# Performance work log

Hardware: AMD Instinct MI355X
Metric: run time of the kernel (lower is better)

Reference implementation:

```python
import jax, jax.numpy as jnp
import numpy as np

B, L, H, HKV, D, E = 2, 2048, 8, 1, 256, 2048
SCALING = D ** -0.5


def rotate_half(x):
    x1, x2 = jnp.split(x, 2, axis=-1)
    return jnp.concatenate([-x2, x1], axis=-1)


def setup_inputs() -> dict:
    key = jax.random.key(0)
    ks = jax.random.split(key, 5)
    hidden_states = jax.random.normal(ks[0], (B, L, E), jnp.float32)
    attention_mask = jnp.zeros((B, 1, 1, L, L), jnp.float32)  # additive mask (all visible)
    # standard RoPE tables, shape [L, D]
    inv_freq = 1.0 / (10000.0 ** (jnp.arange(0, D, 2, dtype=jnp.float32) / D))
    freqs = jnp.arange(L, dtype=jnp.float32)[:, None] * inv_freq[None, :]
    emb = jnp.concatenate([freqs, freqs], axis=-1)
    cos, sin = jnp.cos(emb), jnp.sin(emb)
    s = 0.02
    Wq = jax.random.normal(ks[1], (H * D, E), jnp.float32) * s
    Wk = jax.random.normal(ks[2], (HKV * D, E), jnp.float32) * s
    Wv = jax.random.normal(ks[3], (HKV * D, E), jnp.float32) * s
    Wo = jax.random.normal(ks[4], (E, H * D), jnp.float32) * s
    return {"hidden_states": hidden_states, "attention_mask": attention_mask,
            "cos": cos, "sin": sin, "Wq": Wq, "Wk": Wk, "Wv": Wv, "Wo": Wo}


def reference(hidden_states, attention_mask, cos, sin, Wq, Wk, Wv, Wo):
    b, l, _ = hidden_states.shape
    q = jnp.einsum('ble,de->bld', hidden_states, Wq)
    k = jnp.einsum('ble,de->bld', hidden_states, Wk)
    v = jnp.einsum('ble,de->bld', hidden_states, Wv)
    # q: [B, L, 1, H, D] -> transpose(1,3) -> [B, H, 1, L, D]
    q = jnp.transpose(q.reshape(b, l, 1, H, D), (0, 3, 2, 1, 4))
    # k, v: [B, 1, L, Hkv, D] -> transpose(2,3) -> [B, 1, Hkv, L, D]
    k = jnp.transpose(k.reshape(b, 1, l, HKV, D), (0, 1, 3, 2, 4))
    v = jnp.transpose(v.reshape(b, 1, l, HKV, D), (0, 1, 3, 2, 4))
    # RoPE (cos/sin broadcast over leading dims)
    q = q * cos + rotate_half(q) * sin
    k = k * cos + rotate_half(k) * sin
    # scores: [B, H, Hkv, L, L]
    attn = jnp.matmul(q, jnp.swapaxes(k, -1, -2)) * SCALING
    attn = attn + attention_mask
    attn = jax.nn.softmax(attn.astype(jnp.float32), axis=-1)
    out = jnp.matmul(attn, v)                         # [B, H, Hkv, L, D]
    out = jnp.transpose(out, (0, 1, 3, 2, 4))         # [B, H, L, Hkv, D]
    out = out.reshape(b, l, H * D)                    # row-major reshape, as torch .reshape
    return jnp.einsum('bld,ed->ble', out, Wo)
```

## Files before the change

### kernel.cpp

```cpp
#include <hip/hip_runtime.h>

typedef unsigned short u16;
typedef __attribute__((ext_vector_type(8))) short short8;
typedef __attribute__((ext_vector_type(4))) float f32x4;
typedef __attribute__((ext_vector_type(16))) float f32x16;

struct __align__(8) US4 { u16 x, y, z, w; };

__device__ __forceinline__ u16 f2bf(float x) {
  union { float f; unsigned u; } c; c.f = x;
  unsigned r = c.u + 0x7fffu + ((c.u >> 16) & 1u);
  return (u16)(r >> 16);
}
__device__ __forceinline__ float bf2f(u16 u) {
  union { unsigned u; float f; } c; c.u = ((unsigned)u) << 16;
  return c.f;
}
__device__ __forceinline__ void gload_lds16(const void* g, void* l) {
  __builtin_amdgcn_global_load_lds(
      (const __attribute__((address_space(1))) void*)g,
      (__attribute__((address_space(3))) void*)l, 16, 0, 0);
}
__device__ __forceinline__ f32x4 fzero4() {
  f32x4 z; z[0] = 0.f; z[1] = 0.f; z[2] = 0.f; z[3] = 0.f; return z;
}
__device__ __forceinline__ unsigned cvtpk(float lo, float hi) {
  unsigned r;
  asm("v_cvt_pk_bf16_f32 %0, %1, %2" : "=v"(r) : "v"(lo), "v"(hi));
  return r;
}

__global__ __launch_bounds__(256) void cvt_all(
    const float* __restrict__ h, const float* __restrict__ wq,
    const float* __restrict__ wk, const float* __restrict__ wv,
    const float* __restrict__ wo, u16* __restrict__ Xbf,
    u16* __restrict__ Wqkv, u16* __restrict__ Wob) {
  int b = blockIdx.x;
  const float* s; u16* d; int off;
  if (b < 8192)       { s = h;  d = Xbf;            off = b; }
  else if (b < 12288) { s = wq; d = Wqkv;           off = b - 8192; }
  else if (b < 12800) { s = wk; d = Wqkv + 4194304; off = b - 12288; }
  else if (b < 13312) { s = wv; d = Wqkv + 4718592; off = b - 12800; }
  else                { s = wo; d = Wob;            off = b - 13312; }
  int i = (off * 256 + threadIdx.x) * 4;
  float4 v = *(const float4*)(s + i);
  US4 o = { f2bf(v.x), f2bf(v.y), f2bf(v.z), f2bf(v.w) };
  *(US4*)(d + i) = o;
}

template <int MODE>
__global__ __launch_bounds__(256) void gemm_nt(
    const u16* __restrict__ A, const u16* __restrict__ Bw,
    u16* __restrict__ q_out, u16* __restrict__ k_out, u16* __restrict__ v_out,
    float* __restrict__ c_out) {
  __shared__ u16 lA[128 * 32];
  __shared__ u16 lB[128 * 32];
  const int K = 2048;
  int t = threadIdx.x, w = t >> 6, lane = t & 63;
  int wm = w >> 1, wn = w & 1;

  int gx = gridDim.x;
  int wg = blockIdx.y * gx + blockIdx.x;
  int per = (gx * gridDim.y) >> 3;
  int nid = (wg & 7) * per + (wg >> 3);
  int m0 = (nid % gx) * 128, n0 = (nid / gx) * 128;

  int g = lane >> 4, qi = lane & 15;

  f32x4 acc[4][4];
#pragma unroll
  for (int i = 0; i < 4; i++)
#pragma unroll
    for (int j = 0; j < 4; j++) acc[i][j] = fzero4();

  for (int k0 = 0; k0 < K; k0 += 32) {
#pragma unroll
    for (int i = 0; i < 2; i++) {
      int off = i * 4096 + w * 1024 + lane * 16;
      int row = off >> 6, cg = (off >> 4) & 3;
      gload_lds16(A + (size_t)(m0 + row) * K + k0 + cg * 8,
                  (char*)lA + i * 4096 + w * 1024);
      gload_lds16(Bw + (size_t)(n0 + row) * K + k0 + cg * 8,
                  (char*)lB + i * 4096 + w * 1024);
    }
    __syncthreads();
    short8 af[4], bfr[4];
#pragma unroll
    for (int f = 0; f < 4; f++) {
      int ra = wm * 64 + f * 16 + qi;
      int rb = wn * 64 + f * 16 + qi;
      int kb2 = g * 16;
      af[f] = *(const short8*)((const char*)lA + ra * 64 + kb2);
      bfr[f] = *(const short8*)((const char*)lB + rb * 64 + kb2);
    }
#pragma unroll
    for (int i = 0; i < 4; i++)
#pragma unroll
      for (int j = 0; j < 4; j++)
        acc[i][j] = __builtin_amdgcn_mfma_f32_16x16x32_bf16(af[i], bfr[j], acc[i][j], 0, 0, 0);
    __syncthreads();
  }

#pragma unroll
  for (int i = 0; i < 4; i++) {
#pragma unroll
    for (int j = 0; j < 4; j++) {
#pragma unroll
      for (int r = 0; r < 4; r++) {
        int m = m0 + wm * 64 + i * 16 + g * 4 + r;
        int n = n0 + wn * 64 + j * 16 + qi;
        float v = acc[i][j][r];
        if (MODE == 0) {
          int b = m >> 11, l = m & 2047;
          if (n < 2048) {
            int hh = n >> 8, dd = n & 255;
            q_out[(((size_t)(b * 8 + hh) * 2048) + l) * 256 + dd] = f2bf(v);
          } else if (n < 2304) {
            int dd = n - 2048;
            k_out[((size_t)b * 2048 + l) * 256 + dd] = f2bf(v);
          } else {
            int dd = n - 2304;
            v_out[((size_t)b * 256 + dd) * 2048 + l] = f2bf(v);
          }
        } else {
          c_out[(size_t)m * 2048 + n] = v;
        }
      }
    }
  }
}

__global__ __launch_bounds__(256) void rope_kernel(u16* __restrict__ q, u16* __restrict__ k,
                                                   const float* __restrict__ cosT,
                                                   const float* __restrict__ sinT) {
  int idx = blockIdx.x * 2 + (threadIdx.x >> 7);
  int d = threadIdx.x & 127;
  u16* ptr;
  int l;
  float sc;
  if (idx < 32768) { ptr = q + (size_t)idx * 256; l = idx & 2047; sc = 0.0625f; }
  else             { ptr = k + (size_t)(idx - 32768) * 256; l = (idx - 32768) & 2047; sc = 1.0f; }
  float x1 = bf2f(ptr[d]), x2 = bf2f(ptr[d + 128]);
  float c1 = cosT[l * 256 + d], s1 = sinT[l * 256 + d];
  float c2 = cosT[l * 256 + d + 128], s2 = sinT[l * 256 + d + 128];
  float o1 = (x1 * c1 - x2 * s1) * sc;
  float o2 = (x2 * c2 + x1 * s2) * sc;
  ptr[d] = f2bf(o1);
  ptr[d + 128] = f2bf(o2);
}

__global__ __launch_bounds__(256, 2) void flash_kernel(
    const u16* __restrict__ qr, const u16* __restrict__ kr,
    const u16* __restrict__ vt_g, u16* __restrict__ attnout) {
  __shared__ __align__(16) char lds[66560];

  int t = threadIdx.x, w = t >> 6, lane = t & 63;
  int lo5 = lane & 31, hi = lane >> 5;
  int half = w & 1, qsl = w >> 1;
  int b = blockIdx.z, h = blockIdx.y;
  int bh = b * 8 + h;
  int l0 = blockIdx.x * 64;
  int qrow = l0 + qsl * 32 + lo5;

  const u16* kb = kr + (size_t)b * (2048 * 256);
  const u16* vb = vt_g + (size_t)b * (256 * 2048);
  char* unit = lds + half * 32768;
  int kvbase = half * 1024;

  short8 qf[16];
  {
    const u16* qb = qr + ((size_t)bh * 2048 + qrow) * 256 + hi * 8;
#pragma unroll
    for (int ks = 0; ks < 16; ks++) qf[ks] = *(const short8*)(qb + ks * 16);
  }

  f32x16 ot[8];
#pragma unroll
  for (int dv = 0; dv < 8; dv++)
#pragma unroll
    for (int r = 0; r < 16; r++) ot[dv][r] = 0.f;
  float mrow = -1e30f, lrow = 0.f;

  auto stage = [&](int it) {
    int kvg = kvbase + it * 32;
#pragma unroll
    for (int i = 0; i < 8; i++) {
      int dbase = i * 2048 + qsl * 1024;
      int o = dbase + lane * 16;
      {
        int row = o >> 9, slot = (o >> 4) & 31, ss = slot ^ (row & 7);
        gload_lds16(kb + (size_t)(kvg + row) * 256 + ss * 8, unit + dbase);
      }
      {
        int dd = o >> 6, slot = (o >> 4) & 3, ss = slot ^ ((dd >> 1) & 3);
        gload_lds16(vb + (size_t)dd * 2048 + kvg + ss * 8, unit + 16384 + dbase);
      }
    }
  };

  stage(0);
  __syncthreads();

  for (int it = 0; it < 32; ++it) {
    f32x16 st;
#pragma unroll
    for (int r = 0; r < 16; r++) st[r] = 0.f;
    __builtin_amdgcn_s_setprio(1);
#pragma unroll
    for (int ks = 0; ks < 16; ks++) {
      int ss = (2 * ks + hi) ^ (lo5 & 7);
      short8 kf = *(const short8*)(unit + lo5 * 512 + ss * 16);
      st = __builtin_amdgcn_mfma_f32_32x32x16_bf16(kf, qf[ks], st, 0, 0, 0);
    }
    __builtin_amdgcn_s_setprio(0);

    float tmax = st[0];
#pragma unroll
    for (int r = 1; r < 16; r++) tmax = fmaxf(tmax, st[r]);
    tmax = fmaxf(tmax, __shfl_xor(tmax, 32));
    if (__any(tmax > mrow)) {
      float mnew = fmaxf(mrow, tmax);
      float scale = __expf(mrow - mnew);
#pragma unroll
      for (int dv = 0; dv < 8; dv++)
#pragma unroll
        for (int r = 0; r < 16; r++) ot[dv][r] *= scale;
      lrow *= scale;
      mrow = mnew;
    }
    float tsum = 0.f;
#pragma unroll
    for (int r = 0; r < 16; r++) {
      float p = __expf(st[r] - mrow);
      st[r] = p;
      tsum += p;
    }
    tsum += __shfl_xor(tsum, 32);
    lrow += tsum;

#pragma unroll
    for (int jks = 0; jks < 2; jks++) {
      union { unsigned u[4]; short8 s; } pfu;
      {
        unsigned a0 = cvtpk(st[8 * jks + 0], st[8 * jks + 1]);
        unsigned a1 = cvtpk(st[8 * jks + 2], st[8 * jks + 3]);
        unsigned b0 = cvtpk(st[8 * jks + 4], st[8 * jks + 5]);
        unsigned b1 = cvtpk(st[8 * jks + 6], st[8 * jks + 7]);
        asm("v_permlane32_swap_b32 %0, %1" : "+v"(a0), "+v"(b0));
        asm("v_permlane32_swap_b32 %0, %1" : "+v"(a1), "+v"(b1));
        pfu.u[0] = a0; pfu.u[1] = a1; pfu.u[2] = b0; pfu.u[3] = b1;
      }
      short8 pf = pfu.s;
      __builtin_amdgcn_s_setprio(1);
#pragma unroll
      for (int dv = 0; dv < 8; dv++) {
        int dd = dv * 32 + lo5;
        int ss = (2 * jks + hi) ^ ((dd >> 1) & 3);
        short8 vf = *(const short8*)(unit + 16384 + dd * 64 + ss * 16);
        ot[dv] = __builtin_amdgcn_mfma_f32_32x32x16_bf16(vf, pf, ot[dv], 0, 0, 0);
      }
      __builtin_amdgcn_s_setprio(0);
    }

    __syncthreads();
    if (it < 31) stage(it + 1);
    __syncthreads();
  }

  char* chunk = lds + qsl * 32768;
  float* mlxq = (float*)(lds + 65536) + qsl * 128;
  if (half == 0) {
#pragma unroll
    for (int dv = 0; dv < 8; dv++)
#pragma unroll
      for (int r4 = 0; r4 < 4; r4++) {
        f32x4 v;
        v[0] = ot[dv][4 * r4 + 0]; v[1] = ot[dv][4 * r4 + 1];
        v[2] = ot[dv][4 * r4 + 2]; v[3] = ot[dv][4 * r4 + 3];
        *(f32x4*)(chunk + ((dv * 4 + r4) * 64 + lane) * 16) = v;
      }
    mlxq[lane * 2 + 0] = mrow;
    mlxq[lane * 2 + 1] = lrow;
  }
  __syncthreads();
  if (half == 1) {
    float mA = mlxq[lane * 2 + 0], lA = mlxq[lane * 2 + 1];
    float m = fmaxf(mA, mrow);
    float cA = __expf(mA - m), cB = __expf(mrow - m);
    float linv = 1.f / (lA * cA + lrow * cB);
    u16* ob = attnout + ((size_t)bh * 2048 + qrow) * 256;
#pragma unroll
    for (int dv = 0; dv < 8; dv++)
#pragma unroll
      for (int r4 = 0; r4 < 4; r4++) {
        f32x4 oA = *(const f32x4*)(chunk + ((dv * 4 + r4) * 64 + lane) * 16);
        US4 o;
        o.x = f2bf((oA[0] * cA + ot[dv][4 * r4 + 0] * cB) * linv);
        o.y = f2bf((oA[1] * cA + ot[dv][4 * r4 + 1] * cB) * linv);
        o.z = f2bf((oA[2] * cA + ot[dv][4 * r4 + 2] * cB) * linv);
        o.w = f2bf((oA[3] * cA + ot[dv][4 * r4 + 3] * cB) * linv);
        *(US4*)(ob + dv * 32 + 8 * r4 + 4 * hi) = o;
      }
  }
}

extern "C" void kernel_launch(void* const* d_in, const int* in_sizes, int n_in,
                              void* d_out, int out_size, void* d_ws, size_t ws_size,
                              hipStream_t stream) {
  const float* hidden = (const float*)d_in[0];
  const float* cosT = (const float*)d_in[2];
  const float* sinT = (const float*)d_in[3];
  const float* Wq = (const float*)d_in[4];
  const float* Wk = (const float*)d_in[5];
  const float* Wv = (const float*)d_in[6];
  const float* Wo = (const float*)d_in[7];

  char* ws = (char*)d_ws;
  u16* Xbf  = (u16*)(ws + 0);
  u16* Wqkv = (u16*)(ws + 16777216);
  u16* Wob  = (u16*)(ws + 27262976);
  u16* qbuf = (u16*)(ws + 35651584);
  u16* kbuf = (u16*)(ws + 52428800);
  u16* vT   = (u16*)(ws + 54525952);
  u16* attn = (u16*)(ws + 56623104);
  float* out = (float*)d_out;

  cvt_all<<<17408, 256, 0, stream>>>(hidden, Wq, Wk, Wv, Wo, Xbf, Wqkv, Wob);
  gemm_nt<0><<<dim3(32, 20), 256, 0, stream>>>(Xbf, Wqkv, qbuf, kbuf, vT, nullptr);
  rope_kernel<<<18432, 256, 0, stream>>>(qbuf, kbuf, cosT, sinT);
  flash_kernel<<<dim3(32, 8, 2), 256, 0, stream>>>(qbuf, kbuf, vT, attn);
  gemm_nt<1><<<dim3(32, 16), 256, 0, stream>>>(attn, Wob, nullptr, nullptr, nullptr, out);
}
```

Measured before the change: 304.8 us.

## Pre-swizzle V into MFMA fragment layout and double-buffer K in LDS

The QKV GEMM epilogue now writes V directly in the per-lane MFMA operand order, so the flash kernel loads V fragments straight from global memory into registers and no longer stages them in LDS. The freed LDS space holds a second K buffer. The next K tile is prefetched at the top of each iteration, which removes one of the two barriers per iteration. The cost is V traffic from global/L2 on every iteration in every block, with its latency exposed right before the PV MFMAs, and a scattered store pattern in the GEMM epilogue.

```diff
diff --git a/kernel.cpp b/kernel.cpp
--- a/kernel.cpp
+++ b/kernel.cpp
@@ -120,7 +120,10 @@
             k_out[((size_t)b * 2048 + l) * 256 + dd] = f2bf(v);
           } else {
             int dd = n - 2304;
-            v_out[((size_t)b * 256 + dd) * 2048 + l] = f2bf(v);
+            int kt = l >> 5, jj = (l >> 4) & 1, hh2 = (l >> 3) & 1, e = l & 7;
+            int lane2 = hh2 * 32 + (dd & 31), dv = dd >> 5;
+            v_out[(size_t)b * 524288 +
+                  (((size_t)(kt * 16 + jj * 8 + dv)) << 9) + lane2 * 8 + e] = f2bf(v);
           }
         } else {
           c_out[(size_t)m * 2048 + n] = v;
@@ -151,7 +154,7 @@
 
 __global__ __launch_bounds__(256, 2) void flash_kernel(
     const u16* __restrict__ qr, const u16* __restrict__ kr,
-    const u16* __restrict__ vt_g, u16* __restrict__ attnout) {
+    const u16* __restrict__ vsw, u16* __restrict__ attnout) {
   __shared__ __align__(16) char lds[66560];
 
   int t = threadIdx.x, w = t >> 6, lane = t & 63;
@@ -163,9 +166,9 @@
   int qrow = l0 + qsl * 32 + lo5;
 
   const u16* kb = kr + (size_t)b * (2048 * 256);
-  const u16* vb = vt_g + (size_t)b * (256 * 2048);
-  char* unit = lds + half * 32768;
-  int kvbase = half * 1024;
+  const u16* vb = vsw + (size_t)b * 524288;
+  char* kreg = lds + half * 32768;
+  int kt0 = half * 32;
 
   short8 qf[16];
   {
@@ -181,27 +184,26 @@
     for (int r = 0; r < 16; r++) ot[dv][r] = 0.f;
   float mrow = -1e30f, lrow = 0.f;
 
-  auto stage = [&](int it) {
-    int kvg = kvbase + it * 32;
+  auto stage = [&](int buf, int it) {
+    char* unit = kreg + buf * 16384;
+    int kvg = half * 1024 + it * 32;
 #pragma unroll
     for (int i = 0; i < 8; i++) {
       int dbase = i * 2048 + qsl * 1024;
-      int o = dbase + lane * 16;
-      {
-        int row = o >> 9, slot = (o >> 4) & 31, ss = slot ^ (row & 7);
-        gload_lds16(kb + (size_t)(kvg + row) * 256 + ss * 8, unit + dbase);
-      }
-      {
-        int dd = o >> 6, slot = (o >> 4) & 3, ss = slot ^ ((dd >> 1) & 3);
-        gload_lds16(vb + (size_t)dd * 2048 + kvg + ss * 8, unit + 16384 + dbase);
-      }
+      int off = dbase + lane * 16;
+      int row = off >> 9, slot = (off >> 4) & 31, ss = slot ^ (row & 7);
+      gload_lds16(kb + (size_t)(kvg + row) * 256 + ss * 8, unit + dbase);
     }
   };
 
-  stage(0);
+  stage(0, 0);
   __syncthreads();
 
   for (int it = 0; it < 32; ++it) {
+    int buf = it & 1;
+    if (it < 31) stage(buf ^ 1, it + 1);
+    char* unit = kreg + buf * 16384;
+
     f32x16 st;
 #pragma unroll
     for (int r = 0; r < 16; r++) st[r] = 0.f;
@@ -251,19 +253,16 @@
         pfu.u[0] = a0; pfu.u[1] = a1; pfu.u[2] = b0; pfu.u[3] = b1;
       }
       short8 pf = pfu.s;
+      const u16* vt0 = vb + (((size_t)((kt0 + it) * 16 + jks * 8)) << 9) + lane * 8;
+      short8 vfr[8];
+#pragma unroll
+      for (int dv = 0; dv < 8; dv++) vfr[dv] = *(const short8*)(vt0 + (dv << 9));
       __builtin_amdgcn_s_setprio(1);
 #pragma unroll
-      for (int dv = 0; dv < 8; dv++) {
-        int dd = dv * 32 + lo5;
-        int ss = (2 * jks + hi) ^ ((dd >> 1) & 3);
-        short8 vf = *(const short8*)(unit + 16384 + dd * 64 + ss * 16);
-        ot[dv] = __builtin_amdgcn_mfma_f32_32x32x16_bf16(vf, pf, ot[dv], 0, 0, 0);
-      }
+      for (int dv = 0; dv < 8; dv++)
+        ot[dv] = __builtin_amdgcn_mfma_f32_32x32x16_bf16(vfr[dv], pf, ot[dv], 0, 0, 0);
       __builtin_amdgcn_s_setprio(0);
     }
-
-    __syncthreads();
-    if (it < 31) stage(it + 1);
     __syncthreads();
   }
 
@@ -321,13 +320,13 @@
   u16* Wob  = (u16*)(ws + 27262976);
   u16* qbuf = (u16*)(ws + 35651584);
   u16* kbuf = (u16*)(ws + 52428800);
-  u16* vT   = (u16*)(ws + 54525952);
+  u16* vswz = (u16*)(ws + 54525952);
   u16* attn = (u16*)(ws + 56623104);
   float* out = (float*)d_out;
 
   cvt_all<<<17408, 256, 0, stream>>>(hidden, Wq, Wk, Wv, Wo, Xbf, Wqkv, Wob);
-  gemm_nt<0><<<dim3(32, 20), 256, 0, stream>>>(Xbf, Wqkv, qbuf, kbuf, vT, nullptr);
+  gemm_nt<0><<<dim3(32, 20), 256, 0, stream>>>(Xbf, Wqkv, qbuf, kbuf, vswz, nullptr);
   rope_kernel<<<18432, 256, 0, stream>>>(qbuf, kbuf, cosT, sinT);
-  flash_kernel<<<dim3(32, 8, 2), 256, 0, stream>>>(qbuf, kbuf, vT, attn);
+  flash_kernel<<<dim3(32, 8, 2), 256, 0, stream>>>(qbuf, kbuf, vswz, attn);
   gemm_nt<1><<<dim3(32, 16), 256, 0, stream>>>(attn, Wob, nullptr, nullptr, nullptr, out);
 }
```

Result: faster. 269.8 us (-11.5%).
